# Optimization experiments

Measured on AMD Instinct MI355X. Metric: run time of the kernel, lower is better.

Reference implementation:

```python
import jax, jax.numpy as jnp
import numpy as np

B, S, D, H, F = 2, 2048, 1024, 16, 4096
DH = D // H  # per-head dim = 64
EPS = 1e-5


def _layer_norm(x, g, b):
    mu = jnp.mean(x, axis=-1, keepdims=True)
    var = jnp.mean((x - mu) ** 2, axis=-1, keepdims=True)
    return (x - mu) * jax.lax.rsqrt(var + EPS) * g + b


def _mha(q_in, kv_in, wq, bq, wk, bk, wv, bv, wo, bo, causal):
    b, s, d = q_in.shape
    q = (q_in @ wq + bq).reshape(b, s, H, DH).transpose(0, 2, 1, 3)
    k = (kv_in @ wk + bk).reshape(b, s, H, DH).transpose(0, 2, 1, 3)
    v = (kv_in @ wv + bv).reshape(b, s, H, DH).transpose(0, 2, 1, 3)
    scores = jnp.einsum('bhqd,bhkd->bhqk', q, k) / np.sqrt(DH).astype(np.float32)
    if causal:
        mask = jnp.tril(jnp.ones((s, s), dtype=bool))
        scores = jnp.where(mask, scores, -jnp.inf)
    attn = jax.nn.softmax(scores, axis=-1)
    out = jnp.einsum('bhqk,bhkd->bhqd', attn, v)
    out = out.transpose(0, 2, 1, 3).reshape(b, s, d)
    return out @ wo + bo


def setup_inputs() -> dict:
    key = jax.random.key(0)
    ks = iter(jax.random.split(key, 24))
    def w(shape, fan_in):
        return jax.random.normal(next(ks), shape, jnp.float32) / np.sqrt(fan_in).astype(np.float32)
    inp = {
        'encoder_output': jax.random.normal(next(ks), (B, S, D), jnp.float32),
        'decoder_input': jax.random.normal(next(ks), (B, S, D), jnp.float32),
    }
    for pre in ('sa', 'ca'):
        for nm in ('wq', 'wk', 'wv', 'wo'):
            inp[f'{pre}_{nm}'] = w((D, D), D)
            inp[f'{pre}_b{nm[-1]}'] = jnp.zeros((D,), jnp.float32)
        inp[f'{pre}_g'] = jnp.ones((D,), jnp.float32)
        inp[f'{pre}_bt'] = jnp.zeros((D,), jnp.float32)
    inp['f_w1'] = w((D, F), D); inp['f_b1'] = jnp.zeros((F,), jnp.float32)
    inp['f_w2'] = w((F, D), F); inp['f_b2'] = jnp.zeros((D,), jnp.float32)
    inp['f_g'] = jnp.ones((D,), jnp.float32); inp['f_bt'] = jnp.zeros((D,), jnp.float32)
    return inp


def reference(encoder_output, decoder_input,
              sa_wq, sa_bq, sa_wk, sa_bk, sa_wv, sa_bv, sa_wo, sa_bo, sa_g, sa_bt,
              ca_wq, ca_bq, ca_wk, ca_bk, ca_wv, ca_bv, ca_wo, ca_bo, ca_g, ca_bt,
              f_w1, f_b1, f_w2, f_b2, f_g, f_bt):
    # masked self-attention + residual + LN
    x = _mha(decoder_input, decoder_input, sa_wq, sa_bq, sa_wk, sa_bk, sa_wv, sa_bv, sa_wo, sa_bo, True)
    x = _layer_norm(x + decoder_input, sa_g, sa_bt)
    # encoder-decoder attention + residual + LN
    y = _mha(x, encoder_output, ca_wq, ca_bq, ca_wk, ca_bk, ca_wv, ca_bv, ca_wo, ca_bo, False)
    y = _layer_norm(y + x, ca_g, ca_bt)
    # FFN + residual + LN
    h = jax.nn.relu(y @ f_w1 + f_b1) @ f_w2 + f_b2
    return _layer_norm(h + y, f_g, f_bt)
```

## Files before the change

### kernel.cpp

```cpp
#include <hip/hip_runtime.h>
#include <hip/hip_bf16.h>


typedef __attribute__((ext_vector_type(8))) short bf16x8;
typedef __attribute__((ext_vector_type(4))) float f32x4;
typedef __attribute__((ext_vector_type(16))) float f32x16;

#define LOG2E 1.44269504088896340736f

constexpr int Bb = 2, Ss = 2048, Dd = 1024, Hh = 16, DHd = 64, Ff = 4096;
constexpr int Mrows = Bb * Ss;
constexpr int BHS = Bb * Hh * Ss;

static __device__ __forceinline__ ushort f2b(float f) {
    union { float f; unsigned u; } x{f};
    unsigned r = x.u + 0x7fffu + ((x.u >> 16) & 1u);
    return (ushort)(r >> 16);
}

static __device__ __forceinline__ unsigned pk2(float a, float b) {
    __hip_bfloat162 h = __float22bfloat162_rn(make_float2(a, b));
    unsigned u;
    __builtin_memcpy(&u, &h, 4);
    return u;
}

static __device__ __forceinline__ unsigned pk2t(float a, float b) {
    union { float f; unsigned u; } ua{a}, ub{b};
    return __builtin_amdgcn_perm(ub.u, ua.u, 0x07060302);
}

static __device__ __forceinline__ void gl2lds16(const void* g, void* l) {
    __builtin_amdgcn_global_load_lds(
        (const __attribute__((address_space(1))) void*)g,
        (__attribute__((address_space(3))) void*)l, 16, 0, 0);
}

__global__ __launch_bounds__(256) void cvt_kernel(const float* __restrict__ in,
                                                  ushort* __restrict__ out) {
    int i = (blockIdx.x * 256 + threadIdx.x) * 4;
    float4 v = *(const float4*)(in + i);
    ushort4 u;
    u.x = f2b(v.x); u.y = f2b(v.y); u.z = f2b(v.z); u.w = f2b(v.w);
    *(ushort4*)(out + i) = u;
}

__global__ __launch_bounds__(256) void wtrans_kernel(const float* __restrict__ w,
                                                     ushort* __restrict__ wT,
                                                     int K, int N) {
    __shared__ float t[32][33];
    int tx = threadIdx.x & 31, ty = threadIdx.x >> 5;
    int kb = blockIdx.y * 32, nb = blockIdx.x * 32;
#pragma unroll
    for (int i = 0; i < 4; i++)
        t[ty + i * 8][tx] = w[(size_t)(kb + ty + i * 8) * N + nb + tx];
    __syncthreads();
#pragma unroll
    for (int i = 0; i < 4; i++)
        wT[(size_t)(nb + ty + i * 8) * K + kb + tx] = f2b(t[tx][ty + i * 8]);
}

__global__ __launch_bounds__(256) void pack_bias(const float* __restrict__ a,
                                                 const float* __restrict__ b,
                                                 const float* __restrict__ c,
                                                 float* __restrict__ out) {
    int i = blockIdx.x * 256 + threadIdx.x;
    const float* src = a; int j = i;
    if (i >= 2048)      { src = c; j = i - 2048; }
    else if (i >= 1024) { src = b; j = i - 1024; }
    out[i] = src[j];
}

__global__ __launch_bounds__(256) void gemm_kernel(const ushort* __restrict__ A,
                                                   const ushort* __restrict__ BT,
                                                   const float* __restrict__ bias,
                                                   void* __restrict__ out,
                                                   int M, int N, int K, int klen,
                                                   int mode, int relu, float qsc,
                                                   int vwhich) {
    __shared__ __align__(16) ushort As[128 * 64];
    __shared__ __align__(16) ushort Bs[128 * 64];
    const int tid = threadIdx.x;
    const int lane = tid & 63, wave = tid >> 6;
    const int lr = lane & 15, quad = lane >> 4;
    const int wm = wave & 1, wn = wave >> 1;
    const int nwg = gridDim.x * gridDim.y;
    const int orig = blockIdx.y * gridDim.x + blockIdx.x;
    const int wg = (orig & 7) * (nwg >> 3) + (orig >> 3);
    const int m0 = (wg / gridDim.x) * 128, n0 = (wg % gridDim.x) * 128;
    const int kz = blockIdx.z;
    const int kstart = kz * klen;

    f32x4 acc[4][4];
#pragma unroll
    for (int i = 0; i < 4; i++)
#pragma unroll
        for (int j = 0; j < 4; j++) acc[i][j] = (f32x4){0.f, 0.f, 0.f, 0.f};

    const int srow = tid >> 3;
    const int gchunk = ((tid & 7) ^ (srow & 7)) * 8;
    const ushort* aBase = A + (size_t)(m0 + srow) * K + gchunk;
    const ushort* bBase = BT + (size_t)(n0 + srow) * K + gchunk;
    const size_t rowStep = (size_t)32 * K;

    const int slotA = ((quad) ^ (lr & 7)) * 8;
    const int slotB = ((4 + quad) ^ (lr & 7)) * 8;

    for (int k0 = kstart; k0 < kstart + klen; k0 += 64) {
#pragma unroll
        for (int c = 0; c < 4; c++) {
            gl2lds16(aBase + c * rowStep + k0, &As[c * 2048 + tid * 8]);
            gl2lds16(bBase + c * rowStep + k0, &Bs[c * 2048 + tid * 8]);
        }
        __syncthreads();
#pragma unroll
        for (int kk = 0; kk < 2; kk++) {
            const int slot = kk ? slotB : slotA;
            bf16x8 af[4], bfr[4];
#pragma unroll
            for (int i = 0; i < 4; i++)
                af[i] = *(const bf16x8*)&As[(wm * 64 + i * 16 + lr) * 64 + slot];
#pragma unroll
            for (int j = 0; j < 4; j++)
                bfr[j] = *(const bf16x8*)&Bs[(wn * 64 + j * 16 + lr) * 64 + slot];
#pragma unroll
            for (int i = 0; i < 4; i++)
#pragma unroll
                for (int j = 0; j < 4; j++)
                    acc[i][j] = __builtin_amdgcn_mfma_f32_16x16x32_bf16(af[i], bfr[j], acc[i][j], 0, 0, 0);
        }
        __syncthreads();
    }

#pragma unroll
    for (int j = 0; j < 4; j++) {
        int col = n0 + wn * 64 + j * 16 + lr;
        float bv = (bias && kz == 0) ? bias[col] : 0.f;
#pragma unroll
        for (int i = 0; i < 4; i++) {
            int row0 = m0 + wm * 64 + i * 16 + quad * 4;
            float v[4];
#pragma unroll
            for (int r = 0; r < 4; r++) {
                v[r] = acc[i][j][r] + bv;
                if (relu) v[r] = fmaxf(v[r], 0.f);
            }
            if (mode == 0) {
                float* op = (float*)out + (size_t)kz * M * N;
#pragma unroll
                for (int r = 0; r < 4; r++)
                    op[(size_t)(row0 + r) * N + col] = v[r];
            } else if (mode == 1) {
#pragma unroll
                for (int r = 0; r < 4; r++)
                    ((ushort*)out)[(size_t)(row0 + r) * N + col] = f2b(v[r]);
            } else {
                int which = col >> 10, n1 = col & 1023;
                int h = n1 >> 6, dh = n1 & 63;
                int b = row0 >> 11, s0 = row0 & 2047;
                size_t wbase = (size_t)which * (Bb * Hh * Ss * DHd);
                if (which == vwhich) {
                    uint2 pk;
                    pk.x = pk2(v[0], v[1]); pk.y = pk2(v[2], v[3]);
                    *(uint2*)((ushort*)out + wbase +
                              ((size_t)(b * Hh + h) * DHd + dh) * Ss + s0) = pk;
                } else {
                    float sc = (which == 0) ? qsc : 1.f;
#pragma unroll
                    for (int r = 0; r < 4; r++)
                        ((ushort*)out)[wbase + (((size_t)(b * Hh + h) * Ss + s0 + r) * DHd) + dh] =
                            f2b(v[r] * sc);
                }
            }
        }
    }
}

#define MFMAP(I0)                                                              \
    __builtin_amdgcn_s_setprio(1);                                             \
    _Pragma("unroll")                                                          \
    for (int j = 0; j < 4; j++) {                                              \
        acc[I0][j] = __builtin_amdgcn_mfma_f32_16x16x32_bf16(af[0][0], bfr[j][0], acc[I0][j], 0, 0, 0);         \
        acc[I0][j] = __builtin_amdgcn_mfma_f32_16x16x32_bf16(af[0][1], bfr[j][1], acc[I0][j], 0, 0, 0);         \
        acc[I0 + 1][j] = __builtin_amdgcn_mfma_f32_16x16x32_bf16(af[1][0], bfr[j][0], acc[I0 + 1][j], 0, 0, 0); \
        acc[I0 + 1][j] = __builtin_amdgcn_mfma_f32_16x16x32_bf16(af[1][1], bfr[j][1], acc[I0 + 1][j], 0, 0, 0); \
    }                                                                          \
    __builtin_amdgcn_s_setprio(0);

#define PHASE_READ_A(IB)                                                       \
    af[0][0] = *(const bf16x8*)&Ac[aoff0 + (IB) * 1024];                       \
    af[0][1] = *(const bf16x8*)&Ac[aoff1 + (IB) * 1024];                       \
    af[1][0] = *(const bf16x8*)&Ac[aoff0 + ((IB) + 1) * 1024];                 \
    af[1][1] = *(const bf16x8*)&Ac[aoff1 + ((IB) + 1) * 1024];

#define GTILE(PF)                                                              \
  {                                                                            \
    const ushort* Ac = &As[(t & 1) * 16384];                                   \
    const ushort* Bc = &Bs[(t & 1) * 16384];                                   \
    const int nb = (t & 1) ^ 1;                                                \
    const int kn = kstart + (t + 1) * 64;                                      \
    bf16x8 bfr[4][2], af[2][2];                                                \
                                                        \
    _Pragma("unroll")                                                          \
    for (int j = 0; j < 4; j++) {                                              \
        bfr[j][0] = *(const bf16x8*)&Bc[boff0 + j * 1024];                     \
        bfr[j][1] = *(const bf16x8*)&Bc[boff1 + j * 1024];                     \
    }                                                                          \
    PHASE_READ_A(0)                                                            \
    if (PF) { stB(nb, kn, 0); stB(nb, kn, 1); }                                \
    __builtin_amdgcn_s_barrier();                                              \
    asm volatile("s_waitcnt lgkmcnt(0)" ::: "memory");                         \
    MFMAP(0)                                                                   \
    __builtin_amdgcn_s_barrier();                                              \
                                                        \
    PHASE_READ_A(2)                                                            \
    if (PF) { stB(nb, kn, 2); stB(nb, kn, 3); }                                \
    __builtin_amdgcn_s_barrier();                                              \
    asm volatile("s_waitcnt lgkmcnt(0)" ::: "memory");                         \
    MFMAP(2)                                                                   \
    if (PF) asm volatile("s_waitcnt vmcnt(4)" ::: "memory");                   \
    else    asm volatile("s_waitcnt vmcnt(0)" ::: "memory");                   \
    __builtin_amdgcn_s_barrier();                                              \
                                                        \
    PHASE_READ_A(4)                                                            \
    if (PF) { stA(nb, kn, 0); stA(nb, kn, 2); }                                \
    __builtin_amdgcn_s_barrier();                                              \
    asm volatile("s_waitcnt lgkmcnt(0)" ::: "memory");                         \
    MFMAP(4)                                                                   \
    __builtin_amdgcn_s_barrier();                                              \
                                                        \
    PHASE_READ_A(6)                                                            \
    if (PF) { stA(nb, kn, 1); stA(nb, kn, 3); }                                \
    __builtin_amdgcn_s_barrier();                                              \
    asm volatile("s_waitcnt lgkmcnt(0)" ::: "memory");                         \
    MFMAP(6)                                                                   \
    if (PF) asm volatile("s_waitcnt vmcnt(2)" ::: "memory");                   \
    __builtin_amdgcn_s_barrier();                                              \
  }

__global__ __launch_bounds__(512) void gemm256(const ushort* __restrict__ A,
                                               const ushort* __restrict__ BT,
                                               const float* __restrict__ bias,
                                               void* __restrict__ out,
                                               int M, int N, int K, int klen,
                                               int mode, int relu, float qsc,
                                               int vwhich) {
    __shared__ __align__(16) ushort As[2 * 16384];
    __shared__ __align__(16) ushort Bs[2 * 16384];
    const int tid = threadIdx.x;
    const int lane = tid & 63, wave = tid >> 6;
    const int lr = lane & 15, quad = lane >> 4;
    const int wm = wave & 1, wn = wave >> 1;
    const int nwg = gridDim.x * gridDim.y;
    const int orig = blockIdx.y * gridDim.x + blockIdx.x;
    const int wg = (orig & 7) * (nwg >> 3) + (orig >> 3);
    const int m0 = (wg / gridDim.x) * 256, n0 = (wg % gridDim.x) * 256;
    const int kz = blockIdx.z;
    const int kstart = kz * klen;

    f32x4 acc[8][4];
#pragma unroll
    for (int i = 0; i < 8; i++)
#pragma unroll
        for (int j = 0; j < 4; j++) acc[i][j] = (f32x4){0.f, 0.f, 0.f, 0.f};

    const int srow = tid >> 3;
    const int gchunk = ((tid & 7) ^ (srow & 7)) * 8;
    const ushort* aBase = A + (size_t)(m0 + srow) * K + gchunk;
    const ushort* bBase = BT + (size_t)(n0 + srow) * K + gchunk;
    const size_t rowStep = (size_t)64 * K;

    auto stA = [&](int b, int kn, int c) {
        gl2lds16(aBase + (size_t)c * rowStep + kn, &As[b * 16384 + c * 4096 + tid * 8]);
    };
    auto stB = [&](int b, int kn, int c) {
        gl2lds16(bBase + (size_t)c * rowStep + kn, &Bs[b * 16384 + c * 4096 + tid * 8]);
    };

    const int aoff0 = (wm * 128 + lr) * 64 + (((0 * 4 + quad)) ^ (lr & 7)) * 8;
    const int aoff1 = (wm * 128 + lr) * 64 + (((1 * 4 + quad)) ^ (lr & 7)) * 8;
    const int boff0 = (wn * 64 + lr) * 64 + (((0 * 4 + quad)) ^ (lr & 7)) * 8;
    const int boff1 = (wn * 64 + lr) * 64 + (((1 * 4 + quad)) ^ (lr & 7)) * 8;

    stB(0, kstart, 0); stB(0, kstart, 1); stB(0, kstart, 2); stB(0, kstart, 3);
    stA(0, kstart, 0); stA(0, kstart, 2); stA(0, kstart, 1); stA(0, kstart, 3);
    asm volatile("s_waitcnt vmcnt(2)" ::: "memory");
    __builtin_amdgcn_s_barrier();

    const int nkt = klen >> 6;
    for (int t = 0; t < nkt - 1; t++) GTILE(1)
    { const int t = nkt - 1; GTILE(0) }

#pragma unroll
    for (int j = 0; j < 4; j++) {
        int col = n0 + wn * 64 + j * 16 + lr;
        float bv = (bias && kz == 0) ? bias[col] : 0.f;
#pragma unroll
        for (int i = 0; i < 8; i++) {
            int row0 = m0 + wm * 128 + i * 16 + quad * 4;
            float v[4];
#pragma unroll
            for (int r = 0; r < 4; r++) {
                v[r] = acc[i][j][r] + bv;
                if (relu) v[r] = fmaxf(v[r], 0.f);
            }
            if (mode == 0) {
                float* op = (float*)out + (size_t)kz * M * N;
#pragma unroll
                for (int r = 0; r < 4; r++)
                    op[(size_t)(row0 + r) * N + col] = v[r];
            } else if (mode == 1) {
#pragma unroll
                for (int r = 0; r < 4; r++)
                    ((ushort*)out)[(size_t)(row0 + r) * N + col] = f2b(v[r]);
            } else {
                int which = col >> 10, n1 = col & 1023;
                int h = n1 >> 6, dh = n1 & 63;
                int b = row0 >> 11, s0 = row0 & 2047;
                size_t wbase = (size_t)which * (Bb * Hh * Ss * DHd);
                if (which == vwhich) {
                    uint2 pk;
                    pk.x = pk2(v[0], v[1]); pk.y = pk2(v[2], v[3]);
                    *(uint2*)((ushort*)out + wbase +
                              ((size_t)(b * Hh + h) * DHd + dh) * Ss + s0) = pk;
                } else {
                    float sc = (which == 0) ? qsc : 1.f;
#pragma unroll
                    for (int r = 0; r < 4; r++)
                        ((ushort*)out)[wbase + (((size_t)(b * Hh + h) * Ss + s0 + r) * DHd) + dh] =
                            f2b(v[r] * sc);
                }
            }
        }
    }
}

__global__ __launch_bounds__(256, 2) void attn_kernel(const ushort* __restrict__ Q,
                                                      const ushort* __restrict__ Kg,
                                                      const ushort* __restrict__ VT,
                                                      float* __restrict__ Op0,
                                                      float* __restrict__ Op1,
                                                      float* __restrict__ Ml,
                                                      int causal) {
    __shared__ __align__(16) ushort Ks[2][64 * 64];
    __shared__ __align__(16) ushort Vs[2][64 * 64];
    const int tid = threadIdx.x;
    const int lane = tid & 63, w = tid >> 6;
    const int lr31 = lane & 31, hi = lane >> 5, l7 = lane & 7;
    const int hi4 = hi * 4;
    const int L = blockIdx.z * 256 + blockIdx.y * 8 + blockIdx.x;
    const int bh = (L & 7) | (((L >> 6) & 3) << 3);
    const int bx = (L >> 3) & 7;
    const int p = L >> 8;
    const int qt = causal ? (p ? bx : (7 - bx)) : bx;
    const size_t hb = (size_t)bh * Ss * DHd;
    const int qbase = qt * 256 + w * 64;

    bf16x8 qf[2][4];
#pragma unroll
    for (int qg = 0; qg < 2; qg++)
#pragma unroll
        for (int ks = 0; ks < 4; ks++)
            qf[qg][ks] = *(const bf16x8*)(Q + hb +
                (size_t)(qbase + qg * 32 + lr31) * DHd + ks * 16 + hi * 8);

    f32x16 o[2][2];
#pragma unroll
    for (int i = 0; i < 2; i++)
#pragma unroll
        for (int j = 0; j < 2; j++)
#pragma unroll
            for (int r = 0; r < 16; r++) o[i][j][r] = 0.f;
    float l0 = 0.f, l1 = 0.f;

    const int srow8 = tid >> 3, sslot = tid & 7;
    const int sswz = (sslot ^ (srow8 & 7)) * 8;
    const ushort* kSrc = Kg + hb + (size_t)srow8 * DHd + sswz;
    const ushort* vSrc = VT + hb + (size_t)srow8 * Ss + sswz;

    uint4 kr0, kr1, vr0, vr1;
    auto ldKV = [&](int k0) {
        kr0 = *(const uint4*)(kSrc + (size_t)(k0 +  0) * DHd);
        kr1 = *(const uint4*)(kSrc + (size_t)(k0 + 32) * DHd);
        vr0 = *(const uint4*)(vSrc + k0);
        vr1 = *(const uint4*)(vSrc + (size_t)32 * Ss + k0);
    };
    auto wrKV = [&](int b) {
        *(uint4*)&Ks[b][tid * 8]        = kr0;
        *(uint4*)&Ks[b][2048 + tid * 8] = kr1;
        *(uint4*)&Vs[b][tid * 8]        = vr0;
        *(uint4*)&Vs[b][2048 + tid * 8] = vr1;
    };

    int so[4];
#pragma unroll
    for (int ks = 0; ks < 4; ks++) so[ks] = ((ks * 2 + hi) ^ l7) * 8;

    const int ktEnd = causal ? (qt + 1) * 4 : (Ss / 64);

    ldKV(p * 64);
    wrKV(0);
    if (p + 2 < ktEnd) ldKV((p + 2) * 64);
    __syncthreads();

    int cur = 0;
    for (int kt = p; kt < ktEnd; kt += 2) {
        const int k0 = kt * 64;
        if (kt + 2 < ktEnd) wrKV(cur ^ 1);
        if (kt + 4 < ktEnd) ldKV((kt + 4) * 64);
        const ushort* Kc = Ks[cur];
        const ushort* Vc = Vs[cur];
        if (!causal || k0 <= qbase + 63) {
            bf16x8 pb[2][4];
            float ps0 = 0.f, ps1 = 0.f;
            const int maskT = causal && (k0 == qbase);
#pragma unroll
            for (int kg = 0; kg < 2; kg++) {
                bf16x8 kf[4];
#pragma unroll
                for (int ks = 0; ks < 4; ks++)
                    kf[ks] = *(const bf16x8*)&Kc[(kg * 32 + lr31) * 64 + so[ks]];
                f32x16 st[2];
#pragma unroll
                for (int qg = 0; qg < 2; qg++) {
#pragma unroll
                    for (int r = 0; r < 16; r++) st[qg][r] = 0.f;
                }
                __builtin_amdgcn_s_setprio(1);
#pragma unroll
                for (int qg = 0; qg < 2; qg++) {
#pragma unroll
                    for (int ks = 0; ks < 4; ks++)
                        st[qg] = __builtin_amdgcn_mfma_f32_32x32x16_bf16(
                            kf[ks], qf[qg][ks], st[qg], 0, 0, 0);
                }
                __builtin_amdgcn_s_setprio(0);
                if (maskT) {
#pragma unroll
                    for (int r = 0; r < 16; r++) {
                        int klr = kg * 32 + (r & 3) + 8 * (r >> 2) + hi4;
                        st[0][r] = (klr > lr31) ? -1e30f : st[0][r];
                        st[1][r] = (klr > lr31 + 32) ? -1e30f : st[1][r];
                    }
                }
#pragma unroll
                for (int qg = 0; qg < 2; qg++) {
                    float pv[16];
#pragma unroll
                    for (int r = 0; r < 16; r++) {
                        pv[r] = __builtin_amdgcn_exp2f(st[qg][r]);
                        if (qg == 0) ps0 += pv[r]; else ps1 += pv[r];
                    }
#pragma unroll
                    for (int tt = 0; tt < 2; tt++) {
                        const int rb = tt * 8;
                        unsigned X0 = pk2t(pv[rb + 0], pv[rb + 1]);
                        unsigned X1 = pk2t(pv[rb + 2], pv[rb + 3]);
                        unsigned Y0 = pk2t(pv[rb + 4], pv[rb + 5]);
                        unsigned Y1 = pk2t(pv[rb + 6], pv[rb + 7]);
                        asm("v_permlane32_swap_b32 %0, %1" : "+v"(X0), "+v"(Y0));
                        asm("v_permlane32_swap_b32 %0, %1" : "+v"(X1), "+v"(Y1));
                        union { unsigned u[4]; bf16x8 v; } pw;
                        pw.u[0] = X0; pw.u[1] = X1; pw.u[2] = Y0; pw.u[3] = Y1;
                        pb[qg][kg * 2 + tt] = pw.v;
                    }
                }
            }
            l0 += ps0 + __shfl_xor(ps0, 32);
            l1 += ps1 + __shfl_xor(ps1, 32);
            __builtin_amdgcn_s_setprio(1);
#pragma unroll
            for (int ks = 0; ks < 4; ks++) {
                bf16x8 av0 = *(const bf16x8*)&Vc[lr31 * 64 + so[ks]];
                bf16x8 av1 = *(const bf16x8*)&Vc[(32 + lr31) * 64 + so[ks]];
                o[0][0] = __builtin_amdgcn_mfma_f32_32x32x16_bf16(av0, pb[0][ks], o[0][0], 0, 0, 0);
                o[0][1] = __builtin_amdgcn_mfma_f32_32x32x16_bf16(av1, pb[0][ks], o[0][1], 0, 0, 0);
                o[1][0] = __builtin_amdgcn_mfma_f32_32x32x16_bf16(av0, pb[1][ks], o[1][0], 0, 0, 0);
                o[1][1] = __builtin_amdgcn_mfma_f32_32x32x16_bf16(av1, pb[1][ks], o[1][1], 0, 0, 0);
            }
            __builtin_amdgcn_s_setprio(0);
        }
        __syncthreads();
        cur ^= 1;
    }

    Ml[(size_t)p * BHS + (size_t)bh * Ss + qbase + lane] = (lane & 32) ? l1 : l0;
    float* Op = p ? Op1 : Op0;
#pragma unroll
    for (int qg = 0; qg < 2; qg++) {
        size_t ob = ((size_t)bh * Ss + qbase + qg * 32 + lr31) * 64;
#pragma unroll
        for (int dhg = 0; dhg < 2; dhg++)
#pragma unroll
            for (int rq = 0; rq < 4; rq++) {
                f32x4 t;
#pragma unroll
                for (int c = 0; c < 4; c++) t[c] = o[qg][dhg][rq * 4 + c];
                *(f32x4*)(Op + ob + dhg * 32 + rq * 8 + hi4) = t;
            }
    }
}

__global__ __launch_bounds__(256) void attn_combine(const float* __restrict__ Op0,
                                                    const float* __restrict__ Op1,
                                                    const float* __restrict__ Ml,
                                                    ushort* __restrict__ O) {
    int g = blockIdx.x * 256 + threadIdx.x;
    int q = g >> 4, seg = g & 15;
    float inv = 1.f / (Ml[q] + Ml[BHS + q]);
    f32x4 x = *(const f32x4*)(Op0 + (size_t)q * 64 + seg * 4);
    f32x4 y = *(const f32x4*)(Op1 + (size_t)q * 64 + seg * 4);
    int bh = q >> 11, sq = q & 2047, bb = bh >> 4, h = bh & 15;
    uint2 u;
    u.x = pk2((x[0] + y[0]) * inv, (x[1] + y[1]) * inv);
    u.y = pk2((x[2] + y[2]) * inv, (x[3] + y[3]) * inv);
    *(uint2*)(O + ((size_t)(bb * Ss + sq)) * Dd + h * 64 + seg * 4) = u;
}

__global__ __launch_bounds__(256) void ln_kernel(const float* __restrict__ a0,
                                                 const float* __restrict__ a1,
                                                 const float* __restrict__ a2,
                                                 const float* __restrict__ a3,
                                                 const float* __restrict__ resid,
                                                 const float* __restrict__ g,
                                                 const float* __restrict__ bt,
                                                 float* __restrict__ out32,
                                                 ushort* __restrict__ outb) {
    const int row = blockIdx.x, tid = threadIdx.x;
    const size_t base = (size_t)row * Dd + tid * 4;
    float4 av = *(const float4*)(a0 + base);
    if (a1) { float4 t = *(const float4*)(a1 + base); av.x += t.x; av.y += t.y; av.z += t.z; av.w += t.w; }
    if (a2) { float4 t = *(const float4*)(a2 + base); av.x += t.x; av.y += t.y; av.z += t.z; av.w += t.w; }
    if (a3) { float4 t = *(const float4*)(a3 + base); av.x += t.x; av.y += t.y; av.z += t.z; av.w += t.w; }
    float4 rv = *(const float4*)(resid + base);
    float x0 = av.x + rv.x, x1 = av.y + rv.y, x2 = av.z + rv.z, x3 = av.w + rv.w;
    float s = x0 + x1 + x2 + x3;
    float q = x0 * x0 + x1 * x1 + x2 * x2 + x3 * x3;
#pragma unroll
    for (int off = 1; off <= 32; off <<= 1) {
        s += __shfl_xor(s, off);
        q += __shfl_xor(q, off);
    }
    __shared__ float red[8];
    int wave = tid >> 6, lane = tid & 63;
    if (lane == 0) { red[wave] = s; red[4 + wave] = q; }
    __syncthreads();
    s = red[0] + red[1] + red[2] + red[3];
    q = red[4] + red[5] + red[6] + red[7];
    float mu = s * (1.f / Dd);
    float var = q * (1.f / Dd) - mu * mu;
    float rs = rsqrtf(var + 1e-5f);
    int col = tid * 4;
    float4 gv = *(const float4*)(g + col);
    float4 bv = *(const float4*)(bt + col);
    float y0 = (x0 - mu) * rs * gv.x + bv.x;
    float y1 = (x1 - mu) * rs * gv.y + bv.y;
    float y2 = (x2 - mu) * rs * gv.z + bv.z;
    float y3 = (x3 - mu) * rs * gv.w + bv.w;
    if (out32) *(float4*)(out32 + base) = make_float4(y0, y1, y2, y3);
    if (outb) {
        ushort4 u; u.x = f2b(y0); u.y = f2b(y1); u.z = f2b(y2); u.w = f2b(y3);
        *(ushort4*)(outb + base) = u;
    }
}

constexpr size_t OFF_XB     = 0;
constexpr size_t OFF_ENCB   = OFF_XB     + 8388608;
constexpr size_t OFF_QKVWT  = OFF_ENCB   + 8388608;
constexpr size_t OFF_CAWQT  = OFF_QKVWT  + 6291456;
constexpr size_t OFF_CAKVT  = OFF_CAWQT  + 2097152;
constexpr size_t OFF_SAWOT  = OFF_CAKVT  + 4194304;
constexpr size_t OFF_CAWOT  = OFF_SAWOT  + 2097152;
constexpr size_t OFF_FW1T   = OFF_CAWOT  + 2097152;
constexpr size_t OFF_FW2T   = OFF_FW1T   + 8388608;
constexpr size_t OFF_SABQKV = OFF_FW2T   + 8388608;
constexpr size_t OFF_CABKV  = OFF_SABQKV + 12288;
constexpr size_t OFF_QB     = OFF_CABKV  + 8192;
constexpr size_t OFF_KB     = OFF_QB     + 8388608;
constexpr size_t OFF_VB     = OFF_KB     + 8388608;
constexpr size_t OFF_ATTNO  = OFF_VB     + 8388608;
constexpr size_t OFF_F1     = OFF_ATTNO  + 8388608;
constexpr size_t OFF_F2     = OFF_F1     + 16777216;
constexpr size_t OFF_X1B    = OFF_F2     + 16777216;
constexpr size_t OFF_F3     = OFF_X1B    + 8388608;
constexpr size_t OFF_YB     = OFF_F3     + 16777216;
constexpr size_t OFF_H1B    = OFF_YB     + 8388608;

extern "C" void kernel_launch(void* const* d_in, const int* in_sizes, int n_in,
                              void* d_out, int out_size, void* d_ws, size_t ws_size,
                              hipStream_t stream) {
    const float* enc   = (const float*)d_in[0];
    const float* dec   = (const float*)d_in[1];
    const float* sa_wq = (const float*)d_in[2];
    const float* sa_bq = (const float*)d_in[3];
    const float* sa_wk = (const float*)d_in[4];
    const float* sa_bk = (const float*)d_in[5];
    const float* sa_wv = (const float*)d_in[6];
    const float* sa_bv = (const float*)d_in[7];
    const float* sa_wo = (const float*)d_in[8];
    const float* sa_bo = (const float*)d_in[9];
    const float* sa_g  = (const float*)d_in[10];
    const float* sa_bt = (const float*)d_in[11];
    const float* ca_wq = (const float*)d_in[12];
    const float* ca_bq = (const float*)d_in[13];
    const float* ca_wk = (const float*)d_in[14];
    const float* ca_bk = (const float*)d_in[15];
    const float* ca_wv = (const float*)d_in[16];
    const float* ca_bv = (const float*)d_in[17];
    const float* ca_wo = (const float*)d_in[18];
    const float* ca_bo = (const float*)d_in[19];
    const float* ca_g  = (const float*)d_in[20];
    const float* ca_bt = (const float*)d_in[21];
    const float* f_w1  = (const float*)d_in[22];
    const float* f_b1  = (const float*)d_in[23];
    const float* f_w2  = (const float*)d_in[24];
    const float* f_b2  = (const float*)d_in[25];
    const float* f_g   = (const float*)d_in[26];
    const float* f_bt  = (const float*)d_in[27];

    char* ws = (char*)d_ws;
    ushort* xb     = (ushort*)(ws + OFF_XB);
    ushort* encb   = (ushort*)(ws + OFF_ENCB);
    ushort* qkvwT  = (ushort*)(ws + OFF_QKVWT);
    ushort* cawqT  = (ushort*)(ws + OFF_CAWQT);
    ushort* cakvT  = (ushort*)(ws + OFF_CAKVT);
    ushort* sawoT  = (ushort*)(ws + OFF_SAWOT);
    ushort* cawoT  = (ushort*)(ws + OFF_CAWOT);
    ushort* fw1T   = (ushort*)(ws + OFF_FW1T);
    ushort* fw2T   = (ushort*)(ws + OFF_FW2T);
    float*  sabqkv = (float*)(ws + OFF_SABQKV);
    float*  cabkv  = (float*)(ws + OFF_CABKV);
    ushort* qb     = (ushort*)(ws + OFF_QB);
    ushort* kb     = (ushort*)(ws + OFF_KB);
    ushort* vbt    = (ushort*)(ws + OFF_VB);
    ushort* attno  = (ushort*)(ws + OFF_ATTNO);
    float*  f1     = (float*)(ws + OFF_F1);
    float*  f2     = (float*)(ws + OFF_F2);
    ushort* x1b    = (ushort*)(ws + OFF_X1B);
    float*  x1f    = (float*)(ws + OFF_F3);
    ushort* yb     = (ushort*)(ws + OFF_YB);
    ushort* h1b    = (ushort*)(ws + OFF_H1B);
    float*  yfp    = (float*)(ws + OFF_QB);
    float*  ml     = (float*)(ws + OFF_H1B);

    const float QSC = 0.125f * LOG2E;
    const size_t MN = (size_t)Mrows * Dd;

    cvt_kernel<<<4096, 256, 0, stream>>>(dec, xb);
    cvt_kernel<<<4096, 256, 0, stream>>>(enc, encb);
    dim3 tgDD(32, 32);
    wtrans_kernel<<<tgDD, 256, 0, stream>>>(sa_wq, qkvwT,                 Dd, Dd);
    wtrans_kernel<<<tgDD, 256, 0, stream>>>(sa_wk, qkvwT + 1024 * 1024,   Dd, Dd);
    wtrans_kernel<<<tgDD, 256, 0, stream>>>(sa_wv, qkvwT + 2 * 1024 * 1024, Dd, Dd);
    wtrans_kernel<<<tgDD, 256, 0, stream>>>(sa_wo, sawoT,                 Dd, Dd);
    wtrans_kernel<<<tgDD, 256, 0, stream>>>(ca_wq, cawqT,                 Dd, Dd);
    wtrans_kernel<<<tgDD, 256, 0, stream>>>(ca_wk, cakvT,                 Dd, Dd);
    wtrans_kernel<<<tgDD, 256, 0, stream>>>(ca_wv, cakvT + 1024 * 1024,   Dd, Dd);
    wtrans_kernel<<<tgDD, 256, 0, stream>>>(ca_wo, cawoT,                 Dd, Dd);
    wtrans_kernel<<<dim3(128, 32), 256, 0, stream>>>(f_w1, fw1T, Dd, Ff);
    wtrans_kernel<<<dim3(32, 128), 256, 0, stream>>>(f_w2, fw2T, Ff, Dd);
    pack_bias<<<12, 256, 0, stream>>>(sa_bq, sa_bk, sa_bv, sabqkv);
    pack_bias<<<8, 256, 0, stream>>>(ca_bk, ca_bv, nullptr, cabkv);

    gemm256<<<dim3(12, 16, 1), 512, 0, stream>>>(xb, qkvwT, sabqkv, qb,
                                                 Mrows, 3072, Dd, Dd, 2, 0, QSC, 2);
    attn_kernel<<<dim3(8, 32, 2), 256, 0, stream>>>(qb, kb, vbt, f1, x1f, ml, 1);
    attn_combine<<<4096, 256, 0, stream>>>(f1, x1f, ml, attno);
    gemm_kernel<<<dim3(8, 32, 2), 256, 0, stream>>>(attno, sawoT, sa_bo, f1,
                                                    Mrows, Dd, Dd, 512, 0, 0, 1.f, -1);
    ln_kernel<<<4096, 256, 0, stream>>>(f1, f2, nullptr, nullptr, dec,
                                        sa_g, sa_bt, x1f, x1b);

    gemm_kernel<<<dim3(8, 32, 1), 256, 0, stream>>>(x1b, cawqT, ca_bq, qb,
                                                    Mrows, Dd, Dd, Dd, 2, 0, QSC, -1);
    gemm256<<<dim3(8, 16, 1), 512, 0, stream>>>(encb, cakvT, cabkv, kb,
                                                Mrows, 2048, Dd, Dd, 2, 0, 1.f, 1);
    attn_kernel<<<dim3(8, 32, 2), 256, 0, stream>>>(qb, kb, vbt, f1, f2, ml, 0);
    attn_combine<<<4096, 256, 0, stream>>>(f1, f2, ml, attno);
    gemm_kernel<<<dim3(8, 32, 2), 256, 0, stream>>>(attno, cawoT, ca_bo, f1,
                                                    Mrows, Dd, Dd, 512, 0, 0, 1.f, -1);
    ln_kernel<<<4096, 256, 0, stream>>>(f1, f2, nullptr, nullptr, x1f,
                                        ca_g, ca_bt, yfp, yb);

    gemm256<<<dim3(16, 16, 1), 512, 0, stream>>>(yb, fw1T, f_b1, h1b,
                                                 Mrows, Ff, Dd, Dd, 1, 1, 1.f, -1);
    gemm256<<<dim3(4, 16, 4), 512, 0, stream>>>(h1b, fw2T, f_b2, f1,
                                                Mrows, Dd, Ff, 1024, 0, 0, 1.f, -1);
    ln_kernel<<<4096, 256, 0, stream>>>(f1, f1 + MN, f1 + 2 * MN, f1 + 3 * MN, yfp,
                                        f_g, f_bt, (float*)d_out, nullptr);
}
```

Measured before the change: 569.7 us.

## Store split-K GEMM partials in bf16 and batch setup kernels

Split-K GEMM partial sums for the output projections and FFN down-projection are now written as bf16 instead of fp32. A new layer-norm variant reads and sums those bf16 partials, which halves the traffic for the partial buffers. The small setup launches (two input conversions, eight square weight transposes, two bias packs) are merged into fewer kernels to cut launch overhead. Rounding each partial to bf16 before the reduction adds precision loss.

```diff
diff --git a/kernel.cpp b/kernel.cpp
--- a/kernel.cpp
+++ b/kernel.cpp
@@ -16,6 +16,11 @@
     union { float f; unsigned u; } x{f};
     unsigned r = x.u + 0x7fffu + ((x.u >> 16) & 1u);
     return (ushort)(r >> 16);
+}
+
+static __device__ __forceinline__ float b2f(ushort u) {
+    union { unsigned u; float f; } x{(unsigned)u << 16};
+    return x.f;
 }
 
 static __device__ __forceinline__ unsigned pk2(float a, float b) {
@@ -36,13 +41,17 @@
         (__attribute__((address_space(3))) void*)l, 16, 0, 0);
 }
 
-__global__ __launch_bounds__(256) void cvt_kernel(const float* __restrict__ in,
-                                                  ushort* __restrict__ out) {
+__global__ __launch_bounds__(256) void cvt2_kernel(const float* __restrict__ a,
+                                                   const float* __restrict__ b,
+                                                   ushort* __restrict__ oa,
+                                                   ushort* __restrict__ ob) {
     int i = (blockIdx.x * 256 + threadIdx.x) * 4;
-    float4 v = *(const float4*)(in + i);
+    const float* src = a; ushort* dst = oa; int j = i;
+    if (i >= 4194304) { src = b; dst = ob; j = i - 4194304; }
+    float4 v = *(const float4*)(src + j);
     ushort4 u;
     u.x = f2b(v.x); u.y = f2b(v.y); u.z = f2b(v.z); u.w = f2b(v.w);
-    *(ushort4*)(out + i) = u;
+    *(ushort4*)(dst + j) = u;
 }
 
 __global__ __launch_bounds__(256) void wtrans_kernel(const float* __restrict__ w,
@@ -60,15 +69,55 @@
         wT[(size_t)(nb + ty + i * 8) * K + kb + tx] = f2b(t[tx][ty + i * 8]);
 }
 
-__global__ __launch_bounds__(256) void pack_bias(const float* __restrict__ a,
-                                                 const float* __restrict__ b,
-                                                 const float* __restrict__ c,
-                                                 float* __restrict__ out) {
+__global__ __launch_bounds__(256) void wtrans8_kernel(
+        const float* __restrict__ s0, const float* __restrict__ s1,
+        const float* __restrict__ s2, const float* __restrict__ s3,
+        const float* __restrict__ s4, const float* __restrict__ s5,
+        const float* __restrict__ s6, const float* __restrict__ s7,
+        ushort* __restrict__ d0, ushort* __restrict__ d1,
+        ushort* __restrict__ d2, ushort* __restrict__ d3,
+        ushort* __restrict__ d4, ushort* __restrict__ d5,
+        ushort* __restrict__ d6, ushort* __restrict__ d7) {
+    const float* w; ushort* wT;
+    switch (blockIdx.z) {
+        case 0: w = s0; wT = d0; break;
+        case 1: w = s1; wT = d1; break;
+        case 2: w = s2; wT = d2; break;
+        case 3: w = s3; wT = d3; break;
+        case 4: w = s4; wT = d4; break;
+        case 5: w = s5; wT = d5; break;
+        case 6: w = s6; wT = d6; break;
+        default: w = s7; wT = d7; break;
+    }
+    __shared__ float t[32][33];
+    int tx = threadIdx.x & 31, ty = threadIdx.x >> 5;
+    int kb = blockIdx.y * 32, nb = blockIdx.x * 32;
+#pragma unroll
+    for (int i = 0; i < 4; i++)
+        t[ty + i * 8][tx] = w[(size_t)(kb + ty + i * 8) * 1024 + nb + tx];
+    __syncthreads();
+#pragma unroll
+    for (int i = 0; i < 4; i++)
+        wT[(size_t)(nb + ty + i * 8) * 1024 + kb + tx] = f2b(t[tx][ty + i * 8]);
+}
+
+__global__ __launch_bounds__(256) void pack_bias2(const float* __restrict__ qa,
+                                                  const float* __restrict__ qb_,
+                                                  const float* __restrict__ qc,
+                                                  const float* __restrict__ ka,
+                                                  const float* __restrict__ kb_,
+                                                  float* __restrict__ outq,
+                                                  float* __restrict__ outk) {
     int i = blockIdx.x * 256 + threadIdx.x;
-    const float* src = a; int j = i;
-    if (i >= 2048)      { src = c; j = i - 2048; }
-    else if (i >= 1024) { src = b; j = i - 1024; }
-    out[i] = src[j];
+    if (i < 3072) {
+        const float* src = qa; int j = i;
+        if (i >= 2048)      { src = qc; j = i - 2048; }
+        else if (i >= 1024) { src = qb_; j = i - 1024; }
+        outq[i] = src[j];
+    } else {
+        int j = i - 3072;
+        outk[j] = (j < 1024) ? ka[j] : kb_[j - 1024];
+    }
 }
 
 __global__ __launch_bounds__(256) void gemm_kernel(const ushort* __restrict__ A,
@@ -154,6 +203,11 @@
 #pragma unroll
                 for (int r = 0; r < 4; r++)
                     ((ushort*)out)[(size_t)(row0 + r) * N + col] = f2b(v[r]);
+            } else if (mode == 3) {
+                ushort* op = (ushort*)out + (size_t)kz * M * N;
+#pragma unroll
+                for (int r = 0; r < 4; r++)
+                    op[(size_t)(row0 + r) * N + col] = f2b(v[r]);
             } else {
                 int which = col >> 10, n1 = col & 1023;
                 int h = n1 >> 6, dh = n1 & 63;
@@ -313,6 +367,11 @@
 #pragma unroll
                 for (int r = 0; r < 4; r++)
                     ((ushort*)out)[(size_t)(row0 + r) * N + col] = f2b(v[r]);
+            } else if (mode == 3) {
+                ushort* op = (ushort*)out + (size_t)kz * M * N;
+#pragma unroll
+                for (int r = 0; r < 4; r++)
+                    op[(size_t)(row0 + r) * N + col] = f2b(v[r]);
             } else {
                 int which = col >> 10, n1 = col & 1023;
                 int h = n1 >> 6, dh = n1 & 63;
@@ -534,6 +593,57 @@
     if (a3) { float4 t = *(const float4*)(a3 + base); av.x += t.x; av.y += t.y; av.z += t.z; av.w += t.w; }
     float4 rv = *(const float4*)(resid + base);
     float x0 = av.x + rv.x, x1 = av.y + rv.y, x2 = av.z + rv.z, x3 = av.w + rv.w;
+    float s = x0 + x1 + x2 + x3;
+    float q = x0 * x0 + x1 * x1 + x2 * x2 + x3 * x3;
+#pragma unroll
+    for (int off = 1; off <= 32; off <<= 1) {
+        s += __shfl_xor(s, off);
+        q += __shfl_xor(q, off);
+    }
+    __shared__ float red[8];
+    int wave = tid >> 6, lane = tid & 63;
+    if (lane == 0) { red[wave] = s; red[4 + wave] = q; }
+    __syncthreads();
+    s = red[0] + red[1] + red[2] + red[3];
+    q = red[4] + red[5] + red[6] + red[7];
+    float mu = s * (1.f / Dd);
+    float var = q * (1.f / Dd) - mu * mu;
+    float rs = rsqrtf(var + 1e-5f);
+    int col = tid * 4;
+    float4 gv = *(const float4*)(g + col);
+    float4 bv = *(const float4*)(bt + col);
+    float y0 = (x0 - mu) * rs * gv.x + bv.x;
+    float y1 = (x1 - mu) * rs * gv.y + bv.y;
+    float y2 = (x2 - mu) * rs * gv.z + bv.z;
+    float y3 = (x3 - mu) * rs * gv.w + bv.w;
+    if (out32) *(float4*)(out32 + base) = make_float4(y0, y1, y2, y3);
+    if (outb) {
+        ushort4 u; u.x = f2b(y0); u.y = f2b(y1); u.z = f2b(y2); u.w = f2b(y3);
+        *(ushort4*)(outb + base) = u;
+    }
+}
+
+__global__ __launch_bounds__(256) void ln_kernel_b(const ushort* __restrict__ a0,
+                                                   const ushort* __restrict__ a1,
+                                                   const ushort* __restrict__ a2,
+                                                   const ushort* __restrict__ a3,
+                                                   const float* __restrict__ resid,
+                                                   const float* __restrict__ g,
+                                                   const float* __restrict__ bt,
+                                                   float* __restrict__ out32,
+                                                   ushort* __restrict__ outb) {
+    const int row = blockIdx.x, tid = threadIdx.x;
+    const size_t base = (size_t)row * Dd + tid * 4;
+    ushort4 u0 = *(const ushort4*)(a0 + base);
+    float ax = b2f(u0.x), ay = b2f(u0.y), az = b2f(u0.z), aw = b2f(u0.w);
+    if (a1) { ushort4 t = *(const ushort4*)(a1 + base);
+        ax += b2f(t.x); ay += b2f(t.y); az += b2f(t.z); aw += b2f(t.w); }
+    if (a2) { ushort4 t = *(const ushort4*)(a2 + base);
+        ax += b2f(t.x); ay += b2f(t.y); az += b2f(t.z); aw += b2f(t.w); }
+    if (a3) { ushort4 t = *(const ushort4*)(a3 + base);
+        ax += b2f(t.x); ay += b2f(t.y); az += b2f(t.z); aw += b2f(t.w); }
+    float4 rv = *(const float4*)(resid + base);
+    float x0 = ax + rv.x, x1 = ay + rv.y, x2 = az + rv.z, x3 = aw + rv.w;
     float s = x0 + x1 + x2 + x3;
     float q = x0 * x0 + x1 * x1 + x2 * x2 + x3 * x3;
 #pragma unroll
@@ -636,6 +746,7 @@
     ushort* attno  = (ushort*)(ws + OFF_ATTNO);
     float*  f1     = (float*)(ws + OFF_F1);
     float*  f2     = (float*)(ws + OFF_F2);
+    ushort* f1b    = (ushort*)(ws + OFF_F1);
     ushort* x1b    = (ushort*)(ws + OFF_X1B);
     float*  x1f    = (float*)(ws + OFF_F3);
     ushort* yb     = (ushort*)(ws + OFF_YB);
@@ -646,30 +757,24 @@
     const float QSC = 0.125f * LOG2E;
     const size_t MN = (size_t)Mrows * Dd;
 
-    cvt_kernel<<<4096, 256, 0, stream>>>(dec, xb);
-    cvt_kernel<<<4096, 256, 0, stream>>>(enc, encb);
-    dim3 tgDD(32, 32);
-    wtrans_kernel<<<tgDD, 256, 0, stream>>>(sa_wq, qkvwT,                 Dd, Dd);
-    wtrans_kernel<<<tgDD, 256, 0, stream>>>(sa_wk, qkvwT + 1024 * 1024,   Dd, Dd);
-    wtrans_kernel<<<tgDD, 256, 0, stream>>>(sa_wv, qkvwT + 2 * 1024 * 1024, Dd, Dd);
-    wtrans_kernel<<<tgDD, 256, 0, stream>>>(sa_wo, sawoT,                 Dd, Dd);
-    wtrans_kernel<<<tgDD, 256, 0, stream>>>(ca_wq, cawqT,                 Dd, Dd);
-    wtrans_kernel<<<tgDD, 256, 0, stream>>>(ca_wk, cakvT,                 Dd, Dd);
-    wtrans_kernel<<<tgDD, 256, 0, stream>>>(ca_wv, cakvT + 1024 * 1024,   Dd, Dd);
-    wtrans_kernel<<<tgDD, 256, 0, stream>>>(ca_wo, cawoT,                 Dd, Dd);
+    cvt2_kernel<<<8192, 256, 0, stream>>>(dec, enc, xb, encb);
+    wtrans8_kernel<<<dim3(32, 32, 8), 256, 0, stream>>>(
+        sa_wq, sa_wk, sa_wv, sa_wo, ca_wq, ca_wk, ca_wv, ca_wo,
+        qkvwT, qkvwT + 1024 * 1024, qkvwT + 2 * 1024 * 1024, sawoT,
+        cawqT, cakvT, cakvT + 1024 * 1024, cawoT);
     wtrans_kernel<<<dim3(128, 32), 256, 0, stream>>>(f_w1, fw1T, Dd, Ff);
     wtrans_kernel<<<dim3(32, 128), 256, 0, stream>>>(f_w2, fw2T, Ff, Dd);
-    pack_bias<<<12, 256, 0, stream>>>(sa_bq, sa_bk, sa_bv, sabqkv);
-    pack_bias<<<8, 256, 0, stream>>>(ca_bk, ca_bv, nullptr, cabkv);
+    pack_bias2<<<20, 256, 0, stream>>>(sa_bq, sa_bk, sa_bv, ca_bk, ca_bv,
+                                       sabqkv, cabkv);
 
     gemm256<<<dim3(12, 16, 1), 512, 0, stream>>>(xb, qkvwT, sabqkv, qb,
                                                  Mrows, 3072, Dd, Dd, 2, 0, QSC, 2);
     attn_kernel<<<dim3(8, 32, 2), 256, 0, stream>>>(qb, kb, vbt, f1, x1f, ml, 1);
     attn_combine<<<4096, 256, 0, stream>>>(f1, x1f, ml, attno);
-    gemm_kernel<<<dim3(8, 32, 2), 256, 0, stream>>>(attno, sawoT, sa_bo, f1,
-                                                    Mrows, Dd, Dd, 512, 0, 0, 1.f, -1);
-    ln_kernel<<<4096, 256, 0, stream>>>(f1, f2, nullptr, nullptr, dec,
-                                        sa_g, sa_bt, x1f, x1b);
+    gemm_kernel<<<dim3(8, 32, 2), 256, 0, stream>>>(attno, sawoT, sa_bo, f1b,
+                                                    Mrows, Dd, Dd, 512, 3, 0, 1.f, -1);
+    ln_kernel_b<<<4096, 256, 0, stream>>>(f1b, f1b + MN, nullptr, nullptr, dec,
+                                          sa_g, sa_bt, x1f, x1b);
 
     gemm_kernel<<<dim3(8, 32, 1), 256, 0, stream>>>(x1b, cawqT, ca_bq, qb,
                                                     Mrows, Dd, Dd, Dd, 2, 0, QSC, -1);
@@ -677,15 +782,15 @@
                                                 Mrows, 2048, Dd, Dd, 2, 0, 1.f, 1);
     attn_kernel<<<dim3(8, 32, 2), 256, 0, stream>>>(qb, kb, vbt, f1, f2, ml, 0);
     attn_combine<<<4096, 256, 0, stream>>>(f1, f2, ml, attno);
-    gemm_kernel<<<dim3(8, 32, 2), 256, 0, stream>>>(attno, cawoT, ca_bo, f1,
-                                                    Mrows, Dd, Dd, 512, 0, 0, 1.f, -1);
-    ln_kernel<<<4096, 256, 0, stream>>>(f1, f2, nullptr, nullptr, x1f,
-                                        ca_g, ca_bt, yfp, yb);
+    gemm_kernel<<<dim3(8, 32, 2), 256, 0, stream>>>(attno, cawoT, ca_bo, f1b,
+                                                    Mrows, Dd, Dd, 512, 3, 0, 1.f, -1);
+    ln_kernel_b<<<4096, 256, 0, stream>>>(f1b, f1b + MN, nullptr, nullptr, x1f,
+                                          ca_g, ca_bt, yfp, yb);
 
     gemm256<<<dim3(16, 16, 1), 512, 0, stream>>>(yb, fw1T, f_b1, h1b,
                                                  Mrows, Ff, Dd, Dd, 1, 1, 1.f, -1);
-    gemm256<<<dim3(4, 16, 4), 512, 0, stream>>>(h1b, fw2T, f_b2, f1,
-                                                Mrows, Dd, Ff, 1024, 0, 0, 1.f, -1);
-    ln_kernel<<<4096, 256, 0, stream>>>(f1, f1 + MN, f1 + 2 * MN, f1 + 3 * MN, yfp,
-                                        f_g, f_bt, (float*)d_out, nullptr);
-}
+    gemm256<<<dim3(4, 16, 4), 512, 0, stream>>>(h1b, fw2T, f_b2, f1b,
+                                                Mrows, Dd, Ff, 1024, 3, 0, 1.f, -1);
+    ln_kernel_b<<<4096, 256, 0, stream>>>(f1b, f1b + MN, f1b + 2 * MN, f1b + 3 * MN,
+                                          yfp, f_g, f_bt, (float*)d_out, nullptr);
+}
```

After: 541.0 us. 5.0% less time.
